# Kernel tuning notes

Measured on AMD Instinct MI355X. Metric: run time of the kernel, lower is better.

Reference implementation:

```python
import jax, jax.numpy as jnp
import numpy as np

N_NODES = 50000
N_EDGES = 800000
IN_FEAT = 96
NUM_CLASSES = 40
K_HOPS = 2        # SGConv K=2
LPA_ITERS = 3     # lpaiters


def setup_inputs() -> dict:
    key = jax.random.key(0)
    ks = jax.random.split(key, 6)
    x = jax.random.normal(ks[0], (N_NODES, IN_FEAT), dtype=jnp.float32)
    edge_index = jax.random.randint(ks[1], (2, N_EDGES), 0, N_NODES, dtype=jnp.int64)
    y = jax.random.randint(ks[2], (N_NODES,), 0, NUM_CLASSES, dtype=jnp.int64)
    mask = jax.random.bernoulli(ks[3], 0.5, (N_NODES,))
    edge_weight = jnp.ones((N_EDGES,), dtype=jnp.float32)  # nn.Parameter(torch.ones(num_edges))
    W = jax.random.normal(ks[4], (IN_FEAT, NUM_CLASSES), dtype=jnp.float32) / np.sqrt(IN_FEAT)
    b = jax.random.normal(ks[5], (NUM_CLASSES,), dtype=jnp.float32) * 0.01
    return {"x": x, "edge_index": edge_index, "y": y, "mask": mask,
            "edge_weight": edge_weight, "W": W, "b": b}


def _gcn_norm_self_loops(edge_index, edge_weight, n):
    # PyG gcn_norm with add_self_loops=True (SGConv default), fill_value=1
    row, col = edge_index[0], edge_index[1]
    loop = jnp.arange(n, dtype=row.dtype)
    row = jnp.concatenate([row, loop])
    col = jnp.concatenate([col, loop])
    w = jnp.concatenate([edge_weight, jnp.ones((n,), edge_weight.dtype)])
    deg = jax.ops.segment_sum(w, col, num_segments=n)
    dinv = jnp.where(deg > 0, deg ** -0.5, 0.0)
    return row, col, dinv[row] * w * dinv[col]


def _propagate(h, row, col, w, n):
    # gather -> weight -> scatter-add (aggr='add' at target nodes)
    return jax.ops.segment_sum(w[:, None] * h[row], col, num_segments=n)


def reference(x, edge_index, y, mask, edge_weight, W, b):
    n = x.shape[0]
    # ---- SGConv(K=2) with learnable edge_weight, gcn_norm with self-loops ----
    row, col, norm = _gcn_norm_self_loops(edge_index, edge_weight, n)
    h = x
    for _ in range(K_HOPS):
        h = _propagate(h, row, col, norm, n)
    x_out = h @ W + b
    # ---- LPAconv: edge_weight given, so NO gcn_norm; raw weighted scatter-add ----
    y1h = jax.nn.one_hot(y, NUM_CLASSES, dtype=jnp.float32)
    out = jnp.where(mask[:, None], y1h, 0.0)  # out[mask] = y[mask]
    r2, c2 = edge_index[0], edge_index[1]
    for _ in range(LPA_ITERS):
        out = _propagate(out, r2, c2, edge_weight, n)
    return (x_out, out)
```

## Files before the change

### kernel.cpp

```cpp
#include <hip/hip_runtime.h>
#include <hip/hip_fp16.h>

constexpr int N_NODES     = 50000;
constexpr int N_EDGES     = 800000;
constexpr int IN_FEAT     = 96;
constexpr int NUM_CLASSES = 40;
constexpr int CCH = NUM_CLASSES / 4;
constexpr int CH8 = NUM_CLASSES / 8;
constexpr int HS  = 64;
constexpr int CS  = 128;
constexpr int LS  = 64;
constexpr int SCAN_B = 1024;
constexpr int NSCAN = (N_NODES + SCAN_B - 1) / SCAN_B;

__device__ __forceinline__ void h8_to_f(const uint4& u, float4& lo, float4& hi) {
    float2 f0 = __half22float2(*reinterpret_cast<const __half2*>(&u.x));
    float2 f1 = __half22float2(*reinterpret_cast<const __half2*>(&u.y));
    float2 f2 = __half22float2(*reinterpret_cast<const __half2*>(&u.z));
    float2 f3 = __half22float2(*reinterpret_cast<const __half2*>(&u.w));
    lo = make_float4(f0.x, f0.y, f1.x, f1.y);
    hi = make_float4(f2.x, f2.y, f3.x, f3.y);
}
__device__ __forceinline__ uint4 f_to_h8(const float4& lo, const float4& hi) {
    uint4 u;
    *reinterpret_cast<__half2*>(&u.x) = __floats2half2_rn(lo.x, lo.y);
    *reinterpret_cast<__half2*>(&u.y) = __floats2half2_rn(lo.z, lo.w);
    *reinterpret_cast<__half2*>(&u.z) = __floats2half2_rn(hi.x, hi.y);
    *reinterpret_cast<__half2*>(&u.w) = __floats2half2_rn(hi.z, hi.w);
    return u;
}

__global__ void rank_k(const int* __restrict__ col, int* __restrict__ cnt,
                       int* __restrict__ rank) {
    int t = blockIdx.x * blockDim.x + threadIdx.x;
    if (t >= N_EDGES / 8) return;
    int4 c0 = reinterpret_cast<const int4*>(col)[2 * t];
    int4 c1 = reinterpret_cast<const int4*>(col)[2 * t + 1];
    int4 r0, r1;
    r0.x = atomicAdd(&cnt[c0.x], 1);
    r0.y = atomicAdd(&cnt[c0.y], 1);
    r0.z = atomicAdd(&cnt[c0.z], 1);
    r0.w = atomicAdd(&cnt[c0.w], 1);
    r1.x = atomicAdd(&cnt[c1.x], 1);
    r1.y = atomicAdd(&cnt[c1.y], 1);
    r1.z = atomicAdd(&cnt[c1.z], 1);
    r1.w = atomicAdd(&cnt[c1.w], 1);
    reinterpret_cast<int4*>(rank)[2 * t]     = r0;
    reinterpret_cast<int4*>(rank)[2 * t + 1] = r1;
}

__global__ __launch_bounds__(SCAN_B) void scan1_k(const int* __restrict__ cnt,
                                                  int* __restrict__ pscan,
                                                  int* __restrict__ bsum) {
    __shared__ int buf[SCAN_B];
    int tid = threadIdx.x;
    int i = blockIdx.x * SCAN_B + tid;
    int v = (i < N_NODES) ? cnt[i] : 0;
    buf[tid] = v;
    __syncthreads();
    for (int off = 1; off < SCAN_B; off <<= 1) {
        int t = (tid >= off) ? buf[tid - off] : 0;
        __syncthreads();
        buf[tid] += t;
        __syncthreads();
    }
    if (i < N_NODES) pscan[i] = buf[tid] - v;
    if (tid == SCAN_B - 1) bsum[blockIdx.x] = buf[tid];
}

__global__ void scan2_k(const int* __restrict__ bsum, int* __restrict__ boff,
                        int* __restrict__ rowptr) {
    __shared__ int buf[64];
    int tid = threadIdx.x;
    int v = (tid < NSCAN) ? bsum[tid] : 0;
    buf[tid] = v;
    __syncthreads();
    for (int off = 1; off < 64; off <<= 1) {
        int t = (tid >= off) ? buf[tid - off] : 0;
        __syncthreads();
        buf[tid] += t;
        __syncthreads();
    }
    boff[tid] = buf[tid] - v;
    if (tid == NSCAN - 1) rowptr[N_NODES] = buf[tid];
}

__global__ void scan3_k(const int* __restrict__ pscan, const int* __restrict__ boff,
                        int* __restrict__ rowptr) {
    int i = blockIdx.x * blockDim.x + threadIdx.x;
    if (i < N_NODES) rowptr[i] = boff[i >> 10] + pscan[i];
}

__global__ void fill_k(const int* __restrict__ row, const int* __restrict__ col,
                       const float* __restrict__ ew, const int* __restrict__ rowptr,
                       const int* __restrict__ rank, int2* __restrict__ pair) {
    int t = blockIdx.x * blockDim.x + threadIdx.x;
    if (t >= N_EDGES / 4) return;
    int4   c = reinterpret_cast<const int4*>(col)[t];
    int4   r = reinterpret_cast<const int4*>(row)[t];
    int4   k = reinterpret_cast<const int4*>(rank)[t];
    float4 w = reinterpret_cast<const float4*>(ew)[t];
    pair[rowptr[c.x] + k.x] = make_int2(r.x, __float_as_int(w.x));
    pair[rowptr[c.y] + k.y] = make_int2(r.y, __float_as_int(w.y));
    pair[rowptr[c.z] + k.z] = make_int2(r.z, __float_as_int(w.z));
    pair[rowptr[c.w] + k.w] = make_int2(r.w, __float_as_int(w.w));
}

__global__ void node_prep_k(const int* __restrict__ rowptr, const int2* __restrict__ pair,
                            const int* __restrict__ y, const int* __restrict__ mask,
                            unsigned short* __restrict__ xwt) {
    int i = blockIdx.x * blockDim.x + threadIdx.x;
    if (i >= N_NODES) return;
    int p0 = rowptr[i], p1 = rowptr[i + 1];
    float d = 1.0f;
    for (int p = p0; p < p1; ++p) d += __int_as_float(pair[p].y);
    float dv = d > 0.0f ? rsqrtf(d) : 0.0f;
    unsigned short* rowp = xwt + (size_t)i * HS;
    *reinterpret_cast<int*>(rowp + 40)   = (mask[i] != 0) ? y[i] : -1;
    *reinterpret_cast<float*>(rowp + 42) = dv;
}

__global__ __launch_bounds__(256) void xw_k(const float* __restrict__ x,
                                            const float* __restrict__ Wm,
                                            unsigned short* __restrict__ xwt) {
    __shared__ float4 Ws[IN_FEAT * CCH];
    int tid = threadIdx.x;
    for (int t = tid; t < IN_FEAT * CCH; t += 256)
        Ws[t] = reinterpret_cast<const float4*>(Wm)[t];
    __syncthreads();
    int idx = blockIdx.x * 256 + tid;
    if (idx >= N_NODES * CCH) return;
    int i = idx / CCH;
    int j = idx - i * CCH;
    const float4* xr = reinterpret_cast<const float4*>(x + i * IN_FEAT);
    float4 acc = make_float4(0.f, 0.f, 0.f, 0.f);
#pragma unroll
    for (int f4 = 0; f4 < IN_FEAT / 4; ++f4) {
        float4 xv = xr[f4];
        float4 w0 = Ws[(4 * f4 + 0) * CCH + j];
        float4 w1 = Ws[(4 * f4 + 1) * CCH + j];
        float4 w2 = Ws[(4 * f4 + 2) * CCH + j];
        float4 w3 = Ws[(4 * f4 + 3) * CCH + j];
        acc.x = fmaf(xv.x, w0.x, fmaf(xv.y, w1.x, fmaf(xv.z, w2.x, fmaf(xv.w, w3.x, acc.x))));
        acc.y = fmaf(xv.x, w0.y, fmaf(xv.y, w1.y, fmaf(xv.z, w2.y, fmaf(xv.w, w3.y, acc.y))));
        acc.z = fmaf(xv.x, w0.z, fmaf(xv.y, w1.z, fmaf(xv.z, w2.z, fmaf(xv.w, w3.z, acc.z))));
        acc.w = fmaf(xv.x, w0.w, fmaf(xv.y, w1.w, fmaf(xv.z, w2.w, fmaf(xv.w, w3.w, acc.w))));
    }
    uint2 h;
    *reinterpret_cast<__half2*>(&h.x) = __floats2half2_rn(acc.x, acc.y);
    *reinterpret_cast<__half2*>(&h.y) = __floats2half2_rn(acc.z, acc.w);
    reinterpret_cast<uint2*>(xwt + (size_t)i * HS)[j] = h;
}

__global__ void fused1_k(const int* __restrict__ rowptr, const int2* __restrict__ pair,
                         const unsigned short* __restrict__ xwt,
                         unsigned short* __restrict__ comb) {
    int idx = blockIdx.x * blockDim.x + threadIdx.x;
    if (idx >= N_NODES * CH8) return;
    int i = idx / CH8;
    int j = idx - i * CH8;
    int p0 = rowptr[i], p1 = rowptr[i + 1];
    const unsigned short* irow = xwt + (size_t)i * HS;
    float dc = *reinterpret_cast<const float*>(irow + 42);
    float selfw = dc * dc;
    uint4 vh = *reinterpret_cast<const uint4*>(irow + j * 8);
    float4 v0, v1; h8_to_f(vh, v0, v1);
    float4 s0 = make_float4(selfw * v0.x, selfw * v0.y, selfw * v0.z, selfw * v0.w);
    float4 s1 = make_float4(selfw * v1.x, selfw * v1.y, selfw * v1.z, selfw * v1.w);
    float4 a0 = make_float4(0.f, 0.f, 0.f, 0.f);
    float4 a1 = make_float4(0.f, 0.f, 0.f, 0.f);
    int base = j << 3;
    for (int p = p0; p < p1; ++p) {
        int2 pr = pair[p];
        int s = pr.x;
        float w = __int_as_float(pr.y);
        const unsigned short* srow = xwt + (size_t)s * HS;
        uint4 uh = *reinterpret_cast<const uint4*>(srow + j * 8);
        int   t  = *reinterpret_cast<const int*>(srow + 40) - base;
        float ds = *reinterpret_cast<const float*>(srow + 42);
        float nv = ds * (w * dc);
        float4 u0, u1; h8_to_f(uh, u0, u1);
        s0.x = fmaf(nv, u0.x, s0.x); s0.y = fmaf(nv, u0.y, s0.y);
        s0.z = fmaf(nv, u0.z, s0.z); s0.w = fmaf(nv, u0.w, s0.w);
        s1.x = fmaf(nv, u1.x, s1.x); s1.y = fmaf(nv, u1.y, s1.y);
        s1.z = fmaf(nv, u1.z, s1.z); s1.w = fmaf(nv, u1.w, s1.w);
        a0.x += (t == 0) ? w : 0.f; a0.y += (t == 1) ? w : 0.f;
        a0.z += (t == 2) ? w : 0.f; a0.w += (t == 3) ? w : 0.f;
        a1.x += (t == 4) ? w : 0.f; a1.y += (t == 5) ? w : 0.f;
        a1.z += (t == 6) ? w : 0.f; a1.w += (t == 7) ? w : 0.f;
    }
    unsigned short* crow = comb + (size_t)i * CS;
    *reinterpret_cast<uint4*>(crow + j * 8)      = f_to_h8(s0, s1);
    *reinterpret_cast<uint4*>(crow + 40 + j * 8) = f_to_h8(a0, a1);
    if (j == 0) *reinterpret_cast<float*>(crow + 80) = dc;
}

__global__ void fused2_k(const int* __restrict__ rowptr, const int2* __restrict__ pair,
                         const unsigned short* __restrict__ comb,
                         const float* __restrict__ bias,
                         float* __restrict__ out, unsigned short* __restrict__ lBh) {
    int idx = blockIdx.x * blockDim.x + threadIdx.x;
    if (idx >= N_NODES * CH8) return;
    int i = idx / CH8;
    int j = idx - i * CH8;
    int p0 = rowptr[i], p1 = rowptr[i + 1];
    const unsigned short* irow = comb + (size_t)i * CS;
    float dc = *reinterpret_cast<const float*>(irow + 80);
    float selfw = dc * dc;
    uint4 vh = *reinterpret_cast<const uint4*>(irow + j * 8);
    float4 v0, v1; h8_to_f(vh, v0, v1);
    float4 s0 = make_float4(selfw * v0.x, selfw * v0.y, selfw * v0.z, selfw * v0.w);
    float4 s1 = make_float4(selfw * v1.x, selfw * v1.y, selfw * v1.z, selfw * v1.w);
    float4 a0 = make_float4(0.f, 0.f, 0.f, 0.f);
    float4 a1 = make_float4(0.f, 0.f, 0.f, 0.f);
    for (int p = p0; p < p1; ++p) {
        int2 pr = pair[p];
        int s = pr.x;
        float w = __int_as_float(pr.y);
        const unsigned short* srow = comb + (size_t)s * CS;
        uint4 uh = *reinterpret_cast<const uint4*>(srow + j * 8);
        uint4 mh = *reinterpret_cast<const uint4*>(srow + 40 + j * 8);
        float ds = *reinterpret_cast<const float*>(srow + 80);
        float nv = ds * (w * dc);
        float4 u0, u1; h8_to_f(uh, u0, u1);
        float4 m0, m1; h8_to_f(mh, m0, m1);
        s0.x = fmaf(nv, u0.x, s0.x); s0.y = fmaf(nv, u0.y, s0.y);
        s0.z = fmaf(nv, u0.z, s0.z); s0.w = fmaf(nv, u0.w, s0.w);
        s1.x = fmaf(nv, u1.x, s1.x); s1.y = fmaf(nv, u1.y, s1.y);
        s1.z = fmaf(nv, u1.z, s1.z); s1.w = fmaf(nv, u1.w, s1.w);
        a0.x = fmaf(w, m0.x, a0.x); a0.y = fmaf(w, m0.y, a0.y);
        a0.z = fmaf(w, m0.z, a0.z); a0.w = fmaf(w, m0.w, a0.w);
        a1.x = fmaf(w, m1.x, a1.x); a1.y = fmaf(w, m1.y, a1.y);
        a1.z = fmaf(w, m1.z, a1.z); a1.w = fmaf(w, m1.w, a1.w);
    }
    const float4* br = reinterpret_cast<const float4*>(bias) + 2 * j;
    float4 b0 = br[0], b1 = br[1];
    s0.x += b0.x; s0.y += b0.y; s0.z += b0.z; s0.w += b0.w;
    s1.x += b1.x; s1.y += b1.y; s1.z += b1.z; s1.w += b1.w;
    float4* oo = reinterpret_cast<float4*>(out + (size_t)i * NUM_CLASSES) + 2 * j;
    oo[0] = s0; oo[1] = s1;
    *reinterpret_cast<uint4*>(lBh + (size_t)i * LS + j * 8) = f_to_h8(a0, a1);
}

__global__ void lpa3_k(const int* __restrict__ rowptr, const int2* __restrict__ pair,
                       const unsigned short* __restrict__ lBh, float* __restrict__ lout) {
    int idx = blockIdx.x * blockDim.x + threadIdx.x;
    if (idx >= N_NODES * CH8) return;
    int i = idx / CH8;
    int j = idx - i * CH8;
    int p0 = rowptr[i], p1 = rowptr[i + 1];
    float4 a0 = make_float4(0.f, 0.f, 0.f, 0.f);
    float4 a1 = make_float4(0.f, 0.f, 0.f, 0.f);
    for (int p = p0; p < p1; ++p) {
        int2 pr = pair[p];
        int s = pr.x;
        float w = __int_as_float(pr.y);
        uint4 mh = *reinterpret_cast<const uint4*>(lBh + (size_t)s * LS + j * 8);
        float4 m0, m1; h8_to_f(mh, m0, m1);
        a0.x = fmaf(w, m0.x, a0.x); a0.y = fmaf(w, m0.y, a0.y);
        a0.z = fmaf(w, m0.z, a0.z); a0.w = fmaf(w, m0.w, a0.w);
        a1.x = fmaf(w, m1.x, a1.x); a1.y = fmaf(w, m1.y, a1.y);
        a1.z = fmaf(w, m1.z, a1.z); a1.w = fmaf(w, m1.w, a1.w);
    }
    float4* lo = reinterpret_cast<float4*>(lout + (size_t)i * NUM_CLASSES) + 2 * j;
    lo[0] = a0; lo[1] = a1;
}


extern "C" void kernel_launch(void* const* d_in, const int* in_sizes, int n_in,
                              void* d_out, int out_size, void* d_ws, size_t ws_size,
                              hipStream_t stream) {
    const float* x    = (const float*)d_in[0];
    const int*   ei   = (const int*)d_in[1];
    const int*   row  = ei;
    const int*   col  = ei + N_EDGES;
    const int*   y    = (const int*)d_in[2];
    const int*   mask = (const int*)d_in[3];
    const float* ew   = (const float*)d_in[4];
    const float* Wm   = (const float*)d_in[5];
    const float* bias = (const float*)d_in[6];
    float* out     = (float*)d_out;
    float* lpa_out = out + N_NODES * NUM_CLASSES;

    unsigned short* xwt  = (unsigned short*)d_ws;
    unsigned short* comb = xwt + (size_t)N_NODES * HS;
    unsigned short* lBh  = comb + (size_t)N_NODES * CS;
    int2* pair  = (int2*)(lBh + (size_t)N_NODES * LS);
    int* wsi    = (int*)(pair + N_EDGES);
    int* cnt    = wsi;
    int* pscan  = cnt + 50000;
    int* bsum   = pscan + 50048;
    int* boff   = bsum + 64;
    int* rowptr = boff + 64;
    int* rank   = rowptr + 50004;

    const int B = 256;
    auto g = [](long long n, int b) { return (int)((n + b - 1) / b); };

    hipMemsetAsync(cnt, 0, 50000u * sizeof(int), stream);
    rank_k<<<g(N_EDGES / 8, B), B, 0, stream>>>(col, cnt, rank);
    scan1_k<<<NSCAN, SCAN_B, 0, stream>>>(cnt, pscan, bsum);
    scan2_k<<<1, 64, 0, stream>>>(bsum, boff, rowptr);
    scan3_k<<<g(N_NODES, B), B, 0, stream>>>(pscan, boff, rowptr);
    fill_k<<<g(N_EDGES / 4, B), B, 0, stream>>>(row, col, ew, rowptr, rank, pair);

    node_prep_k<<<g(N_NODES, B), B, 0, stream>>>(rowptr, pair, y, mask, xwt);

    xw_k<<<g((long long)N_NODES * CCH, B), B, 0, stream>>>(x, Wm, xwt);

    fused1_k<<<g((long long)N_NODES * CH8, B), B, 0, stream>>>(rowptr, pair, xwt, comb);
    fused2_k<<<g((long long)N_NODES * CH8, B), B, 0, stream>>>(rowptr, pair, comb,
                                                              bias, out, lBh);
    lpa3_k<<<g((long long)N_NODES * CH8, B), B, 0, stream>>>(rowptr, pair, lBh, lpa_out);
}
```

Before: 241.3 us.

## Bucket nodes by in-degree and process gather kernels in degree-sorted order

Builds a degree histogram during node prep, scans it, and produces a permutation that groups nodes of similar in-degree together. The three gather kernels then process nodes in permuted order, so the five threads per node and neighbouring nodes in a wavefront loop over similar edge counts, which is meant to reduce divergence. In exchange it adds two small kernels, a round of atomics, one extra indirection per thread, and less locality for output writes and row reads because consecutive threads now touch scattered nodes.

```diff
diff --git a/kernel.cpp b/kernel.cpp
--- a/kernel.cpp
+++ b/kernel.cpp
@@ -108,7 +108,7 @@
 
 __global__ void node_prep_k(const int* __restrict__ rowptr, const int2* __restrict__ pair,
                             const int* __restrict__ y, const int* __restrict__ mask,
-                            unsigned short* __restrict__ xwt) {
+                            unsigned short* __restrict__ xwt, int* __restrict__ dhist) {
     int i = blockIdx.x * blockDim.x + threadIdx.x;
     if (i >= N_NODES) return;
     int p0 = rowptr[i], p1 = rowptr[i + 1];
@@ -118,6 +118,31 @@
     unsigned short* rowp = xwt + (size_t)i * HS;
     *reinterpret_cast<int*>(rowp + 40)   = (mask[i] != 0) ? y[i] : -1;
     *reinterpret_cast<float*>(rowp + 42) = dv;
+    atomicAdd(&dhist[min(p1 - p0, 63)], 1);
+}
+
+__global__ void bscan_k(const int* __restrict__ dhist, int* __restrict__ bcur) {
+    __shared__ int buf[64];
+    int tid = threadIdx.x;
+    int v = dhist[tid];
+    buf[tid] = v;
+    __syncthreads();
+    for (int off = 1; off < 64; off <<= 1) {
+        int t = (tid >= off) ? buf[tid - off] : 0;
+        __syncthreads();
+        buf[tid] += t;
+        __syncthreads();
+    }
+    bcur[tid] = buf[tid] - v;
+}
+
+__global__ void perm_k(const int* __restrict__ rowptr, int* __restrict__ bcur,
+                       int* __restrict__ perm) {
+    int i = blockIdx.x * blockDim.x + threadIdx.x;
+    if (i >= N_NODES) return;
+    int deg = rowptr[i + 1] - rowptr[i];
+    int pos = atomicAdd(&bcur[min(deg, 63)], 1);
+    perm[pos] = i;
 }
 
 __global__ __launch_bounds__(256) void xw_k(const float* __restrict__ x,
@@ -153,12 +178,13 @@
 }
 
 __global__ void fused1_k(const int* __restrict__ rowptr, const int2* __restrict__ pair,
+                         const int* __restrict__ perm,
                          const unsigned short* __restrict__ xwt,
                          unsigned short* __restrict__ comb) {
     int idx = blockIdx.x * blockDim.x + threadIdx.x;
     if (idx >= N_NODES * CH8) return;
-    int i = idx / CH8;
-    int j = idx - i * CH8;
+    int i = perm[idx / CH8];
+    int j = idx % CH8;
     int p0 = rowptr[i], p1 = rowptr[i + 1];
     const unsigned short* irow = xwt + (size_t)i * HS;
     float dc = *reinterpret_cast<const float*>(irow + 42);
@@ -196,13 +222,14 @@
 }
 
 __global__ void fused2_k(const int* __restrict__ rowptr, const int2* __restrict__ pair,
+                         const int* __restrict__ perm,
                          const unsigned short* __restrict__ comb,
                          const float* __restrict__ bias,
                          float* __restrict__ out, unsigned short* __restrict__ lBh) {
     int idx = blockIdx.x * blockDim.x + threadIdx.x;
     if (idx >= N_NODES * CH8) return;
-    int i = idx / CH8;
-    int j = idx - i * CH8;
+    int i = perm[idx / CH8];
+    int j = idx % CH8;
     int p0 = rowptr[i], p1 = rowptr[i + 1];
     const unsigned short* irow = comb + (size_t)i * CS;
     float dc = *reinterpret_cast<const float*>(irow + 80);
@@ -243,11 +270,12 @@
 }
 
 __global__ void lpa3_k(const int* __restrict__ rowptr, const int2* __restrict__ pair,
+                       const int* __restrict__ perm,
                        const unsigned short* __restrict__ lBh, float* __restrict__ lout) {
     int idx = blockIdx.x * blockDim.x + threadIdx.x;
     if (idx >= N_NODES * CH8) return;
-    int i = idx / CH8;
-    int j = idx - i * CH8;
+    int i = perm[idx / CH8];
+    int j = idx % CH8;
     int p0 = rowptr[i], p1 = rowptr[i + 1];
     float4 a0 = make_float4(0.f, 0.f, 0.f, 0.f);
     float4 a1 = make_float4(0.f, 0.f, 0.f, 0.f);
@@ -288,28 +316,35 @@
     int2* pair  = (int2*)(lBh + (size_t)N_NODES * LS);
     int* wsi    = (int*)(pair + N_EDGES);
     int* cnt    = wsi;
-    int* pscan  = cnt + 50000;
+    int* dhist  = cnt + 50000;
+    int* bcur   = dhist + 64;
+    int* pscan  = bcur + 64;
     int* bsum   = pscan + 50048;
     int* boff   = bsum + 64;
     int* rowptr = boff + 64;
     int* rank   = rowptr + 50004;
+    int* perm   = rank + 800000;
 
     const int B = 256;
     auto g = [](long long n, int b) { return (int)((n + b - 1) / b); };
 
-    hipMemsetAsync(cnt, 0, 50000u * sizeof(int), stream);
+    hipMemsetAsync(cnt, 0, (50000u + 128u) * sizeof(int), stream);
     rank_k<<<g(N_EDGES / 8, B), B, 0, stream>>>(col, cnt, rank);
     scan1_k<<<NSCAN, SCAN_B, 0, stream>>>(cnt, pscan, bsum);
     scan2_k<<<1, 64, 0, stream>>>(bsum, boff, rowptr);
     scan3_k<<<g(N_NODES, B), B, 0, stream>>>(pscan, boff, rowptr);
     fill_k<<<g(N_EDGES / 4, B), B, 0, stream>>>(row, col, ew, rowptr, rank, pair);
 
-    node_prep_k<<<g(N_NODES, B), B, 0, stream>>>(rowptr, pair, y, mask, xwt);
+    node_prep_k<<<g(N_NODES, B), B, 0, stream>>>(rowptr, pair, y, mask, xwt, dhist);
+    bscan_k<<<1, 64, 0, stream>>>(dhist, bcur);
+    perm_k<<<g(N_NODES, B), B, 0, stream>>>(rowptr, bcur, perm);
 
     xw_k<<<g((long long)N_NODES * CCH, B), B, 0, stream>>>(x, Wm, xwt);
 
-    fused1_k<<<g((long long)N_NODES * CH8, B), B, 0, stream>>>(rowptr, pair, xwt, comb);
-    fused2_k<<<g((long long)N_NODES * CH8, B), B, 0, stream>>>(rowptr, pair, comb,
-                                                              bias, out, lBh);
-    lpa3_k<<<g((long long)N_NODES * CH8, B), B, 0, stream>>>(rowptr, pair, lBh, lpa_out);
-}
+    fused1_k<<<g((long long)N_NODES * CH8, B), B, 0, stream>>>(
+        rowptr, pair, perm, xwt, comb);
+    fused2_k<<<g((long long)N_NODES * CH8, B), B, 0, stream>>>(
+        rowptr, pair, perm, comb, bias, out, lBh);
+    lpa3_k<<<g((long long)N_NODES * CH8, B), B, 0, stream>>>(
+        rowptr, pair, perm, lBh, lpa_out);
+}
```

After: 463.4 us. 1.92x slower.
